# Kernel tuning notes

Measured on AMD Instinct MI355X. Metric: run time of the kernel, lower is better.

The kernel has to match this reference:

```python
import jax, jax.numpy as jnp
import numpy as np
import math

_KX = np.array([[1., 0., -1.], [2., 0., -2.], [1., 0., -1.]], dtype=np.float32)
_SOBEL = np.stack([_KX, _KX.T])[:, None]  # (2,1,3,3): gx, gy
_SCALES = [16, 8, 4, 2, 1]
_NBINS = 9


def _hog_layer(x, pw, pb, pool):
    # x: (B,1,H,W); reflect-pad 3x3 Sobel conv -> (B,2,H,W)
    xp = jnp.pad(x, ((0, 0), (0, 0), (1, 1), (1, 1)), mode='reflect')
    gxy = jax.lax.conv_general_dilated(
        xp, jnp.asarray(_SOBEL), (1, 1), 'VALID',
        dimension_numbers=('NCHW', 'OIHW', 'NCHW'))
    gx, gy = gxy[:, 0], gxy[:, 1]
    mag = jnp.sqrt(gx * gx + gy * gy)                       # (B,H,W)
    phase = jnp.arctan2(gx, gy)
    bins = (jnp.floor(phase / math.pi * _NBINS) % _NBINS).astype(jnp.int32)
    # one-hot scatter of magnitude into orientation bins (matches scatter_ on dim 1)
    out = jax.nn.one_hot(bins, _NBINS, dtype=mag.dtype) * mag[..., None]  # (B,H,W,9)
    out = jnp.transpose(out, (0, 3, 1, 2))                  # (B,9,H,W)
    # 1x1 conv with stride=pool == strided slice + channel mix
    o = out[:, :, ::pool, ::pool]
    h = jnp.einsum('oc,nchw->nohw', pw, o) + pb[None, :, None, None]
    nrm = jnp.linalg.norm(h, axis=1, keepdims=True)
    return h / jnp.maximum(nrm, 1e-12)                      # F.normalize(p=2, dim=1)


def _hog_rgb(imgs, pw, pb, pool):
    # run the (shared) HOG layer on R,G,B independently, concat on channel dim
    N, C, H, W = imgs.shape
    h = _hog_layer(imgs.reshape(N * C, 1, H, W), pw, pb, pool)
    return h.reshape(N, C * _NBINS, h.shape[2], h.shape[3])  # (N,27,H/s,W/s)


def _recal_mask(mask, s):
    B, H, W = mask.shape[0], mask.shape[2], mask.shape[3]
    m = mask.astype(jnp.float32).reshape(B, H // s, s, W // s, s)
    return jnp.transpose(m, (0, 1, 3, 2, 4)).mean((-2, -1))  # (B,H/s,W/s)


def _loss(preds, imgs, mask, pws, pbs):
    loss = jnp.float32(0.0)
    for k, s in enumerate(_SCALES):
        tgt = _hog_rgb(imgs, pws[k], pbs[k], s)
        M = _recal_mask(mask, s)
        loss = loss + (((preds[k] - tgt) ** 2).mean(axis=1) * M).sum() / M.sum()
    return loss


def setup_inputs() -> dict:
    key = jax.random.key(0)
    ks = jax.random.split(key, 20)
    N, H, W = 32, 224, 224
    d = {}
    d['imgs'] = jax.random.normal(ks[0], (N, 3, H, W), dtype=jnp.float32)
    d['mask'] = jax.random.uniform(ks[1], (N, 1, H, W), dtype=jnp.float32)
    for k, s in enumerate(_SCALES):
        d['pred%d' % k] = jax.random.normal(ks[2 + k], (N, 27, H // s, W // s), dtype=jnp.float32)
        d['pw%d' % k] = jax.random.normal(ks[7 + k], (9, 9), dtype=jnp.float32) / 3.0
        d['pb%d' % k] = jax.random.normal(ks[12 + k], (9,), dtype=jnp.float32) / 3.0
    return d


def reference(imgs, mask, pred0, pred1, pred2, pred3, pred4,
              pw0, pw1, pw2, pw3, pw4, pb0, pb1, pb2, pb3, pb4):
    preds = [pred0, pred1, pred2, pred3, pred4]
    pws = [pw0, pw1, pw2, pw3, pw4]
    pbs = [pb0, pb1, pb2, pb3, pb4]
    return _loss(preds, imgs, mask, pws, pbs)
```

## Files before the change

### kernel.cpp

```cpp
#include <hip/hip_runtime.h>

#define N_IMG 32
#define H_IMG 224
#define W_IMG 224

#define BS16_END 25
#define BS8_END 123
#define BS4_END 515
#define BS2_END 2083
#define NBLK_TOTAL 5219

__device__ __forceinline__ int reflect_idx(int i, int n) {
    if (i < 0) return -i;
    if (i >= n) return 2 * n - 2 - i;
    return i;
}

__device__ __forceinline__ int bin_from_g(float gx, float gy) {
    float u = gx * __builtin_copysignf(1.0f, gy);
    float w = __builtin_fabsf(gy);
    const float T[9] = {-5.6712818f, -1.7320508f, -0.83909963f, -0.36397023f,
                        0.0f, 0.36397023f, 0.83909963f, 1.7320508f, 5.6712818f};
    int c = 0;
    #pragma unroll
    for (int k = 0; k < 9; ++k) c += (u >= T[k] * w) ? 1 : 0;
    int b = c + 4;
    return (b >= 9) ? b - 9 : b;
}

__device__ __forceinline__ void s1_body2(int rel_bid,
    const float* __restrict__ imgs, const float* __restrict__ mask,
    const float* __restrict__ pred,
    const float* spwT, const float* spb, const float* sA, const float* sB,
    float Cc, float& local, float& mlocal)
{
    constexpr int WsV = W_IMG / 2;
    int vt = rel_bid * 256 + (int)threadIdx.x;
    int jv = vt % WsV;
    int t  = vt / WsV;
    int i  = t % H_IMG;
    int n  = t / H_IMG;
    int j0 = jv * 2;

    constexpr size_t cstride = (size_t)H_IMG * W_IMG;
    float2 mv = *(const float2*)(mask + (size_t)n * cstride + (size_t)i * W_IMG + j0);

    int y0 = reflect_idx(i - 1, H_IMG), y2 = reflect_idx(i + 1, H_IMG);
    int xl = reflect_idx(j0 - 1, W_IMG);
    int xr = reflect_idx(j0 + 2, W_IMG);

    float d2[2] = {0.0f, 0.0f};
    #pragma unroll
    for (int c = 0; c < 3; ++c) {
        const float* im = imgs + (size_t)(n * 3 + c) * cstride;
        const float* q0 = im + (size_t)y0 * W_IMG;
        const float* q1 = im + (size_t)i  * W_IMG;
        const float* q2 = im + (size_t)y2 * W_IMG;

        float r0[4], r1[4], r2[4];
        float2 f;
        r0[0] = q0[xl]; f = *(const float2*)(q0 + j0); r0[1] = f.x; r0[2] = f.y; r0[3] = q0[xr];
        r1[0] = q1[xl]; f = *(const float2*)(q1 + j0); r1[1] = f.x; r1[2] = f.y; r1[3] = q1[xr];
        r2[0] = q2[xl]; f = *(const float2*)(q2 + j0); r2[1] = f.x; r2[2] = f.y; r2[3] = q2[xr];

        const float* pr = pred + ((size_t)(n * 27 + c * 9) * H_IMG + i) * W_IMG + j0;
        float2 p[9];
        #pragma unroll
        for (int o = 0; o < 9; ++o) p[o] = *(const float2*)(pr + o * cstride);

        #pragma unroll
        for (int v = 0; v < 2; ++v) {
            float gx = (r0[v] - r0[v + 2]) + 2.0f * (r1[v] - r1[v + 2]) + (r2[v] - r2[v + 2]);
            float gy = (r0[v] - r2[v]) + 2.0f * (r0[v + 1] - r2[v + 1]) + (r0[v + 2] - r2[v + 2]);
            float mag = sqrtf(gx * gx + gy * gy);
            int bn = bin_from_g(gx, gy);
            float nrm2 = fmaf(mag, fmaf(mag, sA[bn], 2.0f * sB[bn]), Cc);
            float inv = 1.0f / fmaxf(sqrtf(nrm2), 1e-12f);
            #pragma unroll
            for (int o = 0; o < 9; ++o) {
                float h = fmaf(spwT[bn * 9 + o], mag, spb[o]) * inv;
                float pv = (v == 0) ? p[o].x : p[o].y;
                float dd = pv - h;
                d2[v] += dd * dd;
            }
        }
    }

    local  = (mv.x * d2[0] + mv.y * d2[1]) * (1.0f / 27.0f);
    mlocal = mv.x + mv.y;
}

template <int S>
__device__ __forceinline__ void scale_body(int rel_bid,
    const float* __restrict__ imgs, const float* __restrict__ mask,
    const float* __restrict__ pred,
    const float* spwT, const float* spb, const float* sA, const float* sB,
    float Cc, float& local)
{
    constexpr int Hs = H_IMG / S, Ws = W_IMG / S;
    int vt = rel_bid * 256 + (int)threadIdx.x;
    if (vt >= N_IMG * Hs * Ws) return;
    int j = vt % Ws;
    int t = vt / Ws;
    int i = t % Hs;
    int n = t / Hs;

    float M;
    const float* mbase = mask + (size_t)n * H_IMG * W_IMG + (size_t)(i * S) * W_IMG + j * S;
    if constexpr (S == 2) {
        float2 a = *(const float2*)(mbase);
        float2 b = *(const float2*)(mbase + W_IMG);
        M = (a.x + a.y + b.x + b.y) * 0.25f;
    } else {
        float msum = 0.0f;
        #pragma unroll
        for (int a = 0; a < S; ++a) {
            const float* mr = mbase + (size_t)a * W_IMG;
            #pragma unroll
            for (int q = 0; q < S / 4; ++q) {
                float4 fv = *(const float4*)(mr + q * 4);
                msum += (fv.x + fv.y) + (fv.z + fv.w);
            }
        }
        M = msum * (1.0f / (float)(S * S));
    }

    int y = i * S, x = j * S;
    int y0 = reflect_idx(y - 1, H_IMG), y2 = reflect_idx(y + 1, H_IMG);
    int x0 = reflect_idx(x - 1, W_IMG), x2 = reflect_idx(x + 1, W_IMG);
    constexpr size_t cstride = (size_t)Hs * Ws;

    float d2 = 0.0f;
    #pragma unroll
    for (int c = 0; c < 3; ++c) {
        const float* im = imgs + (size_t)(n * 3 + c) * H_IMG * W_IMG;
        const float* q0 = im + (size_t)y0 * W_IMG;
        const float* q1 = im + (size_t)y  * W_IMG;
        const float* q2 = im + (size_t)y2 * W_IMG;
        float p00 = q0[x0], p01 = q0[x], p02 = q0[x2];
        float p10 = q1[x0],             p12 = q1[x2];
        float p20 = q2[x0], p21 = q2[x], p22 = q2[x2];

        const float* pr = pred + ((size_t)(n * 27 + c * 9) * Hs + i) * Ws + j;
        float p[9];
        #pragma unroll
        for (int o = 0; o < 9; ++o) p[o] = pr[o * cstride];

        float gx = (p00 - p02) + 2.0f * (p10 - p12) + (p20 - p22);
        float gy = (p00 - p20) + 2.0f * (p01 - p21) + (p02 - p22);
        float mag = sqrtf(gx * gx + gy * gy);
        int bn = bin_from_g(gx, gy);
        float nrm2 = fmaf(mag, fmaf(mag, sA[bn], 2.0f * sB[bn]), Cc);
        float inv = 1.0f / fmaxf(sqrtf(nrm2), 1e-12f);

        #pragma unroll
        for (int o = 0; o < 9; ++o) {
            float h = fmaf(spwT[bn * 9 + o], mag, spb[o]) * inv;
            float dd = p[o] - h;
            d2 += dd * dd;
        }
    }

    local = M * d2 * (1.0f / 27.0f);
}

__global__ void __launch_bounds__(256) fused_kernel(
    const float* __restrict__ imgs, const float* __restrict__ mask,
    const float* __restrict__ pred0, const float* __restrict__ pred1,
    const float* __restrict__ pred2, const float* __restrict__ pred3,
    const float* __restrict__ pred4,
    const float* __restrict__ pw0, const float* __restrict__ pw1,
    const float* __restrict__ pw2, const float* __restrict__ pw3,
    const float* __restrict__ pw4,
    const float* __restrict__ pb0, const float* __restrict__ pb1,
    const float* __restrict__ pb2, const float* __restrict__ pb3,
    const float* __restrict__ pb4,
    double* __restrict__ pl, double* __restrict__ pm)
{
    __shared__ float spwT[81];
    __shared__ float spb[9];
    __shared__ float sA[9], sB[9], sC[1];

    int bid = blockIdx.x;
    const float* pw;  const float* pb;
    if (bid < BS16_END)      { pw = pw0; pb = pb0; }
    else if (bid < BS8_END)  { pw = pw1; pb = pb1; }
    else if (bid < BS4_END)  { pw = pw2; pb = pb2; }
    else if (bid < BS2_END)  { pw = pw3; pb = pb3; }
    else                     { pw = pw4; pb = pb4; }

    if (threadIdx.x < 81) {
        int o = threadIdx.x / 9, b = threadIdx.x % 9;
        spwT[b * 9 + o] = pw[threadIdx.x];
    }
    if (threadIdx.x < 9) spb[threadIdx.x] = pb[threadIdx.x];
    __syncthreads();
    if (threadIdx.x < 9) {
        float A = 0.0f, B = 0.0f;
        #pragma unroll
        for (int o = 0; o < 9; ++o) {
            float w = spwT[threadIdx.x * 9 + o];
            A += w * w;
            B += w * spb[o];
        }
        sA[threadIdx.x] = A;
        sB[threadIdx.x] = B;
        if (threadIdx.x == 0) {
            float Cc = 0.0f;
            #pragma unroll
            for (int o = 0; o < 9; ++o) Cc += spb[o] * spb[o];
            sC[0] = Cc;
        }
    }
    __syncthreads();
    float Cc = sC[0];

    float local = 0.0f, mlocal = 0.0f;
    if (bid < BS16_END)      scale_body<16>(bid,            imgs, mask, pred0, spwT, spb, sA, sB, Cc, local);
    else if (bid < BS8_END)  scale_body<8>(bid - BS16_END,  imgs, mask, pred1, spwT, spb, sA, sB, Cc, local);
    else if (bid < BS4_END)  scale_body<4>(bid - BS8_END,   imgs, mask, pred2, spwT, spb, sA, sB, Cc, local);
    else if (bid < BS2_END)  scale_body<2>(bid - BS4_END,   imgs, mask, pred3, spwT, spb, sA, sB, Cc, local);
    else                     s1_body2(bid - BS2_END,        imgs, mask, pred4, spwT, spb, sA, sB, Cc, local, mlocal);

    #pragma unroll
    for (int off = 32; off > 0; off >>= 1) {
        local  += __shfl_down(local,  off, 64);
        mlocal += __shfl_down(mlocal, off, 64);
    }
    __shared__ float s1[4], s2[4];
    int lane = threadIdx.x & 63, wid = threadIdx.x >> 6;
    if (lane == 0) { s1[wid] = local; s2[wid] = mlocal; }
    __syncthreads();
    if (threadIdx.x == 0) {
        pl[bid] = (double)(s1[0] + s1[1] + s1[2] + s1[3]);
        pm[bid] = (double)(s2[0] + s2[1] + s2[2] + s2[3]);
    }
}

__global__ void __launch_bounds__(256) finalize_kernel(
    const double* __restrict__ pl, const double* __restrict__ pm,
    float* __restrict__ out)
{
    double l = 0.0, m = 0.0;
    for (int idx = threadIdx.x; idx < NBLK_TOTAL; idx += 256) {
        double w = (idx < BS16_END) ? 256.0 : (idx < BS8_END) ? 64.0
                 : (idx < BS4_END) ? 16.0 : (idx < BS2_END) ? 4.0 : 1.0;
        l += w * pl[idx];
        m += pm[idx];
    }
    #pragma unroll
    for (int off = 32; off > 0; off >>= 1) {
        l += __shfl_down(l, off, 64);
        m += __shfl_down(m, off, 64);
    }
    __shared__ double sl[4], sm[4];
    int lane = threadIdx.x & 63, wid = threadIdx.x >> 6;
    if (lane == 0) { sl[wid] = l; sm[wid] = m; }
    __syncthreads();
    if (threadIdx.x == 0)
        out[0] = (float)((sl[0] + sl[1] + sl[2] + sl[3]) / (sm[0] + sm[1] + sm[2] + sm[3]));
}

extern "C" void kernel_launch(void* const* d_in, const int* in_sizes, int n_in,
                              void* d_out, int out_size, void* d_ws, size_t ws_size,
                              hipStream_t stream) {
    (void)in_sizes; (void)n_in; (void)out_size; (void)ws_size;
    const float* imgs = (const float*)d_in[0];
    const float* mask = (const float*)d_in[1];
    const float* pred[5];
    const float* pw[5];
    const float* pb[5];
    for (int k = 0; k < 5; ++k) {
        pred[k] = (const float*)d_in[2 + 3 * k];
        pw[k]   = (const float*)d_in[3 + 3 * k];
        pb[k]   = (const float*)d_in[4 + 3 * k];
    }
    double* pl = (double*)d_ws;
    double* pm = pl + NBLK_TOTAL;

    fused_kernel<<<NBLK_TOTAL, 256, 0, stream>>>(
        imgs, mask,
        pred[0], pred[1], pred[2], pred[3], pred[4],
        pw[0], pw[1], pw[2], pw[3], pw[4],
        pb[0], pb[1], pb[2], pb[3], pb[4],
        pl, pm);
    finalize_kernel<<<1, 256, 0, stream>>>(pl, pm, (float*)d_out);
}
```

Baseline: 66.08 us.

## Switch fused HOG loss kernel to persistent grid-stride loop over all scales

Measured after the change: 109.9 us. 1.66x slower.

```diff
diff --git a/kernel.cpp b/kernel.cpp
--- a/kernel.cpp
+++ b/kernel.cpp
@@ -4,11 +4,19 @@
 #define H_IMG 224
 #define W_IMG 224
 
-#define BS16_END 25
-#define BS8_END 123
-#define BS4_END 515
-#define BS2_END 2083
-#define NBLK_TOTAL 5219
+#define U16 6272
+#define U8  25088
+#define U4  100352
+#define U2  401408
+#define U1V 802816
+#define O8  (U16)
+#define O4  (O8 + U8)
+#define O2  (O4 + U4)
+#define O1  (O2 + U2)
+#define NTOT (O1 + U1V)
+
+#define NBLK 2048
+#define NTHREADS (NBLK * 256)
 
 __device__ __forceinline__ int reflect_idx(int i, int n) {
     if (i < 0) return -i;
@@ -28,16 +36,15 @@
     return (b >= 9) ? b - 9 : b;
 }
 
-__device__ __forceinline__ void s1_body2(int rel_bid,
+__device__ __forceinline__ float s1_unit(int r,
     const float* __restrict__ imgs, const float* __restrict__ mask,
     const float* __restrict__ pred,
     const float* spwT, const float* spb, const float* sA, const float* sB,
-    float Cc, float& local, float& mlocal)
+    float Cc, float& mout)
 {
     constexpr int WsV = W_IMG / 2;
-    int vt = rel_bid * 256 + (int)threadIdx.x;
-    int jv = vt % WsV;
-    int t  = vt / WsV;
+    int jv = r % WsV;
+    int t  = r / WsV;
     int i  = t % H_IMG;
     int n  = t / H_IMG;
     int j0 = jv * 2;
@@ -86,22 +93,20 @@
         }
     }
 
-    local  = (mv.x * d2[0] + mv.y * d2[1]) * (1.0f / 27.0f);
-    mlocal = mv.x + mv.y;
+    mout = mv.x + mv.y;
+    return (mv.x * d2[0] + mv.y * d2[1]) * (1.0f / 27.0f);
 }
 
 template <int S>
-__device__ __forceinline__ void scale_body(int rel_bid,
+__device__ __forceinline__ float scale_unit(int r,
     const float* __restrict__ imgs, const float* __restrict__ mask,
     const float* __restrict__ pred,
     const float* spwT, const float* spb, const float* sA, const float* sB,
-    float Cc, float& local)
+    float Cc)
 {
     constexpr int Hs = H_IMG / S, Ws = W_IMG / S;
-    int vt = rel_bid * 256 + (int)threadIdx.x;
-    if (vt >= N_IMG * Hs * Ws) return;
-    int j = vt % Ws;
-    int t = vt / Ws;
+    int j = r % Ws;
+    int t = r / Ws;
     int i = t % Hs;
     int n = t / Hs;
 
@@ -161,7 +166,7 @@
         }
     }
 
-    local = M * d2 * (1.0f / 27.0f);
+    return M * d2 * (1.0f / 27.0f);
 }
 
 __global__ void __launch_bounds__(256) fused_kernel(
@@ -177,63 +182,77 @@
     const float* __restrict__ pb4,
     double* __restrict__ pl, double* __restrict__ pm)
 {
-    __shared__ float spwT[81];
-    __shared__ float spb[9];
-    __shared__ float sA[9], sB[9], sC[1];
-
-    int bid = blockIdx.x;
-    const float* pw;  const float* pb;
-    if (bid < BS16_END)      { pw = pw0; pb = pb0; }
-    else if (bid < BS8_END)  { pw = pw1; pb = pb1; }
-    else if (bid < BS4_END)  { pw = pw2; pb = pb2; }
-    else if (bid < BS2_END)  { pw = pw3; pb = pb3; }
-    else                     { pw = pw4; pb = pb4; }
-
-    if (threadIdx.x < 81) {
-        int o = threadIdx.x / 9, b = threadIdx.x % 9;
-        spwT[b * 9 + o] = pw[threadIdx.x];
-    }
-    if (threadIdx.x < 9) spb[threadIdx.x] = pb[threadIdx.x];
+    __shared__ float spwT[5][81];
+    __shared__ float spb[5][9];
+    __shared__ float sA[5][9], sB[5][9], sC[5];
+
+    const float* pws[5] = {pw0, pw1, pw2, pw3, pw4};
+    const float* pbs[5] = {pb0, pb1, pb2, pb3, pb4};
+    #pragma unroll
+    for (int k = 0; k < 5; ++k) {
+        if (threadIdx.x < 81) {
+            int o = threadIdx.x / 9, b = threadIdx.x % 9;
+            spwT[k][b * 9 + o] = pws[k][threadIdx.x];
+        }
+        if (threadIdx.x < 9) spb[k][threadIdx.x] = pbs[k][threadIdx.x];
+    }
     __syncthreads();
-    if (threadIdx.x < 9) {
-        float A = 0.0f, B = 0.0f;
-        #pragma unroll
-        for (int o = 0; o < 9; ++o) {
-            float w = spwT[threadIdx.x * 9 + o];
-            A += w * w;
-            B += w * spb[o];
-        }
-        sA[threadIdx.x] = A;
-        sB[threadIdx.x] = B;
-        if (threadIdx.x == 0) {
-            float Cc = 0.0f;
+    #pragma unroll
+    for (int k = 0; k < 5; ++k) {
+        if (threadIdx.x < 9) {
+            float A = 0.0f, B = 0.0f;
             #pragma unroll
-            for (int o = 0; o < 9; ++o) Cc += spb[o] * spb[o];
-            sC[0] = Cc;
+            for (int o = 0; o < 9; ++o) {
+                float w = spwT[k][threadIdx.x * 9 + o];
+                A += w * w;
+                B += w * spb[k][o];
+            }
+            sA[k][threadIdx.x] = A;
+            sB[k][threadIdx.x] = B;
+            if (threadIdx.x == 0) {
+                float Cv = 0.0f;
+                #pragma unroll
+                for (int o = 0; o < 9; ++o) Cv += spb[k][o] * spb[k][o];
+                sC[k] = Cv;
+            }
         }
     }
     __syncthreads();
-    float Cc = sC[0];
-
-    float local = 0.0f, mlocal = 0.0f;
-    if (bid < BS16_END)      scale_body<16>(bid,            imgs, mask, pred0, spwT, spb, sA, sB, Cc, local);
-    else if (bid < BS8_END)  scale_body<8>(bid - BS16_END,  imgs, mask, pred1, spwT, spb, sA, sB, Cc, local);
-    else if (bid < BS4_END)  scale_body<4>(bid - BS8_END,   imgs, mask, pred2, spwT, spb, sA, sB, Cc, local);
-    else if (bid < BS2_END)  scale_body<2>(bid - BS4_END,   imgs, mask, pred3, spwT, spb, sA, sB, Cc, local);
-    else                     s1_body2(bid - BS2_END,        imgs, mask, pred4, spwT, spb, sA, sB, Cc, local, mlocal);
+
+    float lacc = 0.0f, macc = 0.0f;
+    for (int u = blockIdx.x * 256 + (int)threadIdx.x; u < NTOT; u += NTHREADS) {
+        if (u < O8) {
+            lacc += 256.0f * scale_unit<16>(u, imgs, mask, pred0,
+                        spwT[0], spb[0], sA[0], sB[0], sC[0]);
+        } else if (u < O4) {
+            lacc += 64.0f * scale_unit<8>(u - O8, imgs, mask, pred1,
+                        spwT[1], spb[1], sA[1], sB[1], sC[1]);
+        } else if (u < O2) {
+            lacc += 16.0f * scale_unit<4>(u - O4, imgs, mask, pred2,
+                        spwT[2], spb[2], sA[2], sB[2], sC[2]);
+        } else if (u < O1) {
+            lacc += 4.0f * scale_unit<2>(u - O2, imgs, mask, pred3,
+                        spwT[3], spb[3], sA[3], sB[3], sC[3]);
+        } else {
+            float m;
+            lacc += s1_unit(u - O1, imgs, mask, pred4,
+                        spwT[4], spb[4], sA[4], sB[4], sC[4], m);
+            macc += m;
+        }
+    }
 
     #pragma unroll
     for (int off = 32; off > 0; off >>= 1) {
-        local  += __shfl_down(local,  off, 64);
-        mlocal += __shfl_down(mlocal, off, 64);
-    }
-    __shared__ float s1[4], s2[4];
+        lacc += __shfl_down(lacc, off, 64);
+        macc += __shfl_down(macc, off, 64);
+    }
+    __shared__ float s1s[4], s2s[4];
     int lane = threadIdx.x & 63, wid = threadIdx.x >> 6;
-    if (lane == 0) { s1[wid] = local; s2[wid] = mlocal; }
+    if (lane == 0) { s1s[wid] = lacc; s2s[wid] = macc; }
     __syncthreads();
     if (threadIdx.x == 0) {
-        pl[bid] = (double)(s1[0] + s1[1] + s1[2] + s1[3]);
-        pm[bid] = (double)(s2[0] + s2[1] + s2[2] + s2[3]);
+        pl[blockIdx.x] = (double)(s1s[0] + s1s[1] + s1s[2] + s1s[3]);
+        pm[blockIdx.x] = (double)(s2s[0] + s2s[1] + s2s[2] + s2s[3]);
     }
 }
 
@@ -242,10 +261,8 @@
     float* __restrict__ out)
 {
     double l = 0.0, m = 0.0;
-    for (int idx = threadIdx.x; idx < NBLK_TOTAL; idx += 256) {
-        double w = (idx < BS16_END) ? 256.0 : (idx < BS8_END) ? 64.0
-                 : (idx < BS4_END) ? 16.0 : (idx < BS2_END) ? 4.0 : 1.0;
-        l += w * pl[idx];
+    for (int idx = threadIdx.x; idx < NBLK; idx += 256) {
+        l += pl[idx];
         m += pm[idx];
     }
     #pragma unroll
@@ -276,9 +293,9 @@
         pb[k]   = (const float*)d_in[4 + 3 * k];
     }
     double* pl = (double*)d_ws;
-    double* pm = pl + NBLK_TOTAL;
-
-    fused_kernel<<<NBLK_TOTAL, 256, 0, stream>>>(
+    double* pm = pl + NBLK;
+
+    fused_kernel<<<NBLK, 256, 0, stream>>>(
         imgs, mask,
         pred[0], pred[1], pred[2], pred[3], pred[4],
         pw[0], pw[1], pw[2], pw[3], pw[4],
```
